# Performance work log

Measured on AMD Instinct MI355X. Metric: run time of the kernel, lower is better.

The kernel has to match this reference:

```python
import jax, jax.numpy as jnp
import numpy as np

VOCAB = 32000
LATENT = 1024
HID = 1024
LAYERS = 3
BATCH = 32
MAXLEN = 128


def setup_inputs() -> dict:
    key = jax.random.key(0)
    ks = jax.random.split(key, 10)
    s = 0.02
    return {
        "z": jax.random.normal(ks[0], (BATCH, LATENT), jnp.float32),
        "emb": jax.random.normal(ks[1], (VOCAB, LATENT), jnp.float32) * s,
        "w_lat": jax.random.normal(ks[2], (HID * LAYERS, LATENT), jnp.float32) * s,
        "b_lat": jnp.zeros((HID * LAYERS,), jnp.float32),
        "w_ih": jax.random.normal(ks[3], (LAYERS, 3 * HID, LATENT), jnp.float32) * s,
        "w_hh": jax.random.normal(ks[4], (LAYERS, 3 * HID, HID), jnp.float32) * s,
        "b_ih": jnp.zeros((LAYERS, 3 * HID), jnp.float32),
        "b_hh": jnp.zeros((LAYERS, 3 * HID), jnp.float32),
        "fc_w": jax.random.normal(ks[5], (VOCAB, HID), jnp.float32) * s,
        "fc_b": jnp.zeros((VOCAB,), jnp.float32),
        "max_length": MAXLEN,
    }


def _gru_cell(x, h, w_ih_l, w_hh_l, b_ih_l, b_hh_l):
    # x: [B, in], h: [B, H]; PyTorch GRU gate order: r, z, n
    gx = x @ w_ih_l.T + b_ih_l          # [B, 3H]
    gh = h @ w_hh_l.T + b_hh_l          # [B, 3H]
    xr, xz, xn = jnp.split(gx, 3, axis=-1)
    hr, hz, hn = jnp.split(gh, 3, axis=-1)
    r = jax.nn.sigmoid(xr + hr)
    zg = jax.nn.sigmoid(xz + hz)
    n = jnp.tanh(xn + r * hn)
    return (1.0 - zg) * n + zg * h


def reference(z, emb, w_lat, b_lat, w_ih, w_hh, b_ih, b_hh, fc_w, fc_b, max_length):
    B = z.shape[0]
    L, _, H = w_hh.shape
    # Faithful to source: hidden.view(num_layers, batch, hidden) on a [B, L*H] tensor
    hidden = (z @ w_lat.T + b_lat).reshape(L, B, H)
    tokens0 = jnp.zeros((B,), dtype=jnp.int32)

    def step(carry, _):
        tokens, h = carry
        x = emb[tokens]                          # [B, latent]
        new_h = []
        for l in range(L):                       # small fixed layer loop
            hl = _gru_cell(x, h[l], w_ih[l], w_hh[l], b_ih[l], b_hh[l])
            new_h.append(hl)
            x = hl
        h = jnp.stack(new_h)                     # [L, B, H]
        logits = x @ fc_w.T + fc_b               # [B, V]
        tokens = jnp.argmax(logits, axis=-1).astype(jnp.int32)
        return (tokens, h), logits

    _, logits_seq = jax.lax.scan(step, (tokens0, hidden), None, length=max_length)
    return jnp.transpose(logits_seq, (1, 0, 2))  # [B, T, V]
```

## Files before the change

### kernel.cpp

```cpp
#include <hip/hip_runtime.h>
#include <math.h>
#include <limits.h>

#define B32 32
#define KD 1024
#define HID 1024
#define VOC 32000
#define NL 3
#define TN 128
#define BKC 32
#define ASTR 36
#define WSTR 68
#define GEMM_THREADS 128
#define KS_GRU 4
#define CANDMAX 64

typedef __attribute__((ext_vector_type(8))) short bf16x8;
typedef __attribute__((ext_vector_type(8))) unsigned short u16x8;
typedef __attribute__((ext_vector_type(16))) float f32x16;

__device__ __forceinline__ float sigmoidf_(float x) { return 1.0f / (1.0f + expf(-x)); }

__device__ __forceinline__ unsigned short f2bf(float f) {
    unsigned u = __float_as_uint(f);
    u = u + 0x7fffu + ((u >> 16) & 1u);
    return (unsigned short)(u >> 16);
}
__device__ __forceinline__ float bf2f(unsigned short h) {
    return __uint_as_float(((unsigned)h) << 16);
}
__device__ __forceinline__ f32x16 MF(bf16x8 a, bf16x8 b, f32x16 c) {
    return __builtin_amdgcn_mfma_f32_32x32x16_bf16(a, b, c, 0, 0, 0);
}

__global__ __launch_bounds__(256)
void pack_w(const float* __restrict__ src, unsigned short* __restrict__ hi,
            unsigned short* __restrict__ lo, long ntiles)
{
    long tid = (long)blockIdx.x * 256 + threadIdx.x;
    long total = ntiles * 4096;
    if (tid >= total) return;
    long tile = tid >> 12;
    int r = (int)(tid & 4095);
    int k8 = r >> 5, c = r & 31;
    const float* s = src + ((size_t)tile * 32 + c) * KD + k8 * 8;
    float4 f0 = ((const float4*)s)[0];
    float4 f1 = ((const float4*)s)[1];
    float ff[8] = {f0.x, f0.y, f0.z, f0.w, f1.x, f1.y, f1.z, f1.w};
    u16x8 h, l;
#pragma unroll
    for (int j = 0; j < 8; ++j) {
        unsigned short hh = f2bf(ff[j]);
        h[j] = hh;
        l[j] = f2bf(ff[j] - bf2f(hh));
    }
    size_t o = ((size_t)tile << 15) + (size_t)k8 * 256 + (size_t)c * 8;
    *(u16x8*)(hi + o) = h;
    if (lo) *(u16x8*)(lo + o) = l;
}

__global__ __launch_bounds__(256)
void wnorm_k(const float* __restrict__ fcw, unsigned* __restrict__ wn)
{
    const int tid = threadIdx.x;
    const int r = blockIdx.x * 64 + (tid >> 2);
    const int q = tid & 3;
    const float* row = fcw + (size_t)r * KD + q * 256;
    float s = 0.f;
#pragma unroll 8
    for (int i = 0; i < 64; ++i) {
        float4 v = ((const float4*)row)[i];
        s += v.x * v.x + v.y * v.y + v.z * v.z + v.w * v.w;
    }
    s += __shfl_xor(s, 1);
    s += __shfl_xor(s, 2);
    if (q == 0) atomicMax(wn, __float_as_uint(sqrtf(s)));
}

__global__ __launch_bounds__(256)
void fix_gather(const float* __restrict__ out, int tprev, int T,
                const unsigned short* __restrict__ hh, const unsigned short* __restrict__ hl,
                const float* __restrict__ fcw, const float* __restrict__ fcb,
                const unsigned* __restrict__ wn,
                unsigned long long* __restrict__ wbuf,
                const float* __restrict__ emb,
                unsigned short* __restrict__ xhi, unsigned short* __restrict__ xlo,
                int do_fix)
{
    __shared__ float xs[1024];
    __shared__ float cval[CANDMAX];
    __shared__ int   cand[CANDMAX];
    __shared__ int   lcnt, stok;
    __shared__ float wsum[4];
    __shared__ float sred[4];
    const int b = blockIdx.x, tid = threadIdx.x;
    const int wv = tid >> 6, lane = tid & 63;

    if (do_fix) {
        if (tid == 0) lcnt = 0;
        float sq = 0.f;
        for (int k = tid; k < 1024; k += 256) {
            size_t hp = (size_t)(k >> 3) * 256 + (size_t)b * 8 + (k & 7);
            float xv = bf2f(hh[hp]) + bf2f(hl[hp]);
            xs[k] = xv;
            sq += xv * xv;
        }
#pragma unroll
        for (int m = 1; m < 64; m <<= 1) sq += __shfl_xor(sq, m);
        if (lane == 0) sred[wv] = sq;
        __syncthreads();
        float snorm = sred[0] + sred[1] + sred[2] + sred[3];
        unsigned long long key = wbuf[b];
        unsigned hi32 = (unsigned)(key >> 32);
        unsigned fb = (hi32 & 0x80000000u) ? (hi32 & 0x7fffffffu) : ~hi32;
        float m = __uint_as_float(fb);
        float delta = sqrtf(snorm) * __uint_as_float(wn[0]) * (1.01f / 256.0f) + 1e-7f;
        float thr = m - delta;
        const float* orow = out + ((size_t)b * T + tprev) * VOC;
        for (int i = tid; i < VOC / 4; i += 256) {
            float4 v = ((const float4*)orow)[i];
#pragma unroll
            for (int j = 0; j < 4; ++j) {
                float vv = ((const float*)&v)[j];
                if (vv >= thr) {
                    int pos = atomicAdd(&lcnt, 1);
                    if (pos < CANDMAX) cand[pos] = i * 4 + j;
                }
            }
        }
        __syncthreads();
        int nc = lcnt < CANDMAX ? lcnt : CANDMAX;
        for (int c = 0; c < nc; ++c) {
            const float* wr = fcw + (size_t)cand[c] * KD;
            float p = 0.f;
            for (int k = tid; k < 1024; k += 256) p += xs[k] * wr[k];
#pragma unroll
            for (int mm = 1; mm < 64; mm <<= 1) p += __shfl_xor(p, mm);
            if (lane == 0) wsum[wv] = p;
            __syncthreads();
            if (tid == 0) cval[c] = wsum[0] + wsum[1] + wsum[2] + wsum[3] + fcb[cand[c]];
            __syncthreads();
        }
        if (tid == 0) {
            float bv = -INFINITY; int bi = 0;
            for (int c = 0; c < nc; ++c) {
                float v = cval[c]; int ii = cand[c];
                if (c == 0 || v > bv || (v == bv && ii < bi)) { bv = v; bi = ii; }
            }
            stok = bi;
            wbuf[b] = 0ull;
        }
    }
    __syncthreads();
    int tok = do_fix ? stok : 0;
    if (tid < 128) {
        const float* er = emb + (size_t)tok * KD + (size_t)tid * 8;
        float4 f0 = ((const float4*)er)[0];
        float4 f1 = ((const float4*)er)[1];
        float ff[8] = {f0.x, f0.y, f0.z, f0.w, f1.x, f1.y, f1.z, f1.w};
        u16x8 h, l;
#pragma unroll
        for (int j = 0; j < 8; ++j) {
            unsigned short hv = f2bf(ff[j]);
            h[j] = hv;
            l[j] = f2bf(ff[j] - bf2f(hv));
        }
        size_t o = (size_t)tid * 256 + (size_t)b * 8;
        *(u16x8*)(xhi + o) = h;
        *(u16x8*)(xlo + o) = l;
    }
}

__global__ __launch_bounds__(384)
void gru_gemm(const unsigned short* __restrict__ xhi, const unsigned short* __restrict__ xlo,
              const unsigned short* __restrict__ hhi, const unsigned short* __restrict__ hlo,
              const unsigned short* __restrict__ wihhi, const unsigned short* __restrict__ wihlo,
              const unsigned short* __restrict__ whhhi, const unsigned short* __restrict__ whhlo,
              float* __restrict__ G)
{
    const int bid = blockIdx.x;
    const int jt = bid >> 2, ks4 = bid & 3;
    const int w = threadIdx.x >> 6, lane = threadIdx.x & 63;
    const int gate = (w < 3) ? w : w - 3;
    const unsigned short* Ah = (w < 3) ? xhi : hhi;
    const unsigned short* Al = (w < 3) ? xlo : hlo;
    const size_t woff = ((size_t)(gate * 32 + jt)) << 15;
    const unsigned short* Wh = ((w < 3) ? wihhi : whhhi) + woff;
    const unsigned short* Wl = ((w < 3) ? wihlo : whhlo) + woff;

    const size_t lo8 = (size_t)lane * 8;
    const int kbase = ks4 * 16;

    f32x16 acc = {0,0,0,0,0,0,0,0,0,0,0,0,0,0,0,0};
    bf16x8 ahB[4], alB[4], whB[4], wlB[4];
#pragma unroll
    for (int i = 0; i < 4; ++i) {
        size_t o = (size_t)(kbase + i) * 512 + lo8;
        ahB[i] = *(const bf16x8*)(Ah + o);
        alB[i] = *(const bf16x8*)(Al + o);
        whB[i] = *(const bf16x8*)(Wh + o);
        wlB[i] = *(const bf16x8*)(Wl + o);
    }
#pragma unroll
    for (int i = 0; i < 16; ++i) {
        const int s = i & 3;
        bf16x8 ah = ahB[s], al = alB[s], wh = whB[s], wl = wlB[s];
        if (i < 12) {
            size_t on = (size_t)(kbase + i + 4) * 512 + lo8;
            ahB[s] = *(const bf16x8*)(Ah + on);
            alB[s] = *(const bf16x8*)(Al + on);
            whB[s] = *(const bf16x8*)(Wh + on);
            wlB[s] = *(const bf16x8*)(Wl + on);
        }
        acc = MF(ah, wh, acc);
        acc = MF(al, wh, acc);
        acc = MF(ah, wl, acc);
    }

    const int kg = lane >> 5, c = lane & 31;
    float* Gb = G + (((size_t)(jt * 4 + ks4) * 6 + w) * B32) * 32;
#pragma unroll
    for (int r = 0; r < 16; ++r) {
        int b = (r & 3) + 8 * (r >> 2) + 4 * kg;
        Gb[b * 32 + c] = acc[r];
    }
}

__global__ __launch_bounds__(256)
void gru_gates2(const float* __restrict__ G,
                const float* __restrict__ bih, const float* __restrict__ bhh,
                unsigned short* __restrict__ hhi, unsigned short* __restrict__ hlo)
{
    int idx = blockIdx.x * 256 + threadIdx.x;
    int b = idx >> 10, j = idx & 1023;
    int jt = j >> 5, c = j & 31;
    float s0 = 0, s1 = 0, s2 = 0, s3 = 0, s4 = 0, s5 = 0;
#pragma unroll
    for (int ks = 0; ks < 4; ++ks) {
        const float* base = G + (((size_t)(jt * 4 + ks) * 6) * B32 + b) * 32 + c;
        s0 += base[0];
        s1 += base[1024];
        s2 += base[2048];
        s3 += base[3072];
        s4 += base[4096];
        s5 += base[5120];
    }
    float rg = sigmoidf_(s0 + bih[j] + s3 + bhh[j]);
    float zg = sigmoidf_(s1 + bih[KD + j] + s4 + bhh[KD + j]);
    float ng = tanhf(s2 + bih[2 * KD + j] + rg * (s5 + bhh[2 * KD + j]));
    size_t hp = (size_t)(j >> 3) * 256 + (size_t)b * 8 + (j & 7);
    float hold = bf2f(hhi[hp]) + bf2f(hlo[hp]);
    float hnew = (1.0f - zg) * ng + zg * hold;
    unsigned short hh = f2bf(hnew);
    hhi[hp] = hh;
    hlo[hp] = f2bf(hnew - bf2f(hh));
}

__global__ __launch_bounds__(256)
void logits6(const unsigned short* __restrict__ xh, const unsigned short* __restrict__ xl,
             const unsigned short* __restrict__ wh,
             const float* __restrict__ bias, float* __restrict__ out, int t, int T,
             unsigned long long* __restrict__ wbuf)
{
    __shared__ float bvalS[4][B32];
    __shared__ int   bidxS[4][B32];
    const int tid = threadIdx.x;
    const int w = tid >> 6, lane = tid & 63;
    const int tile = blockIdx.x * 4 + w;
    const int n0 = tile * 32;
    const unsigned short* Wt = wh + ((size_t)tile << 15);
    const size_t lo8 = (size_t)lane * 8;

    f32x16 acc = {0,0,0,0,0,0,0,0,0,0,0,0,0,0,0,0};
    bf16x8 ahB[4], alB[4], wvB[4];
#pragma unroll
    for (int i = 0; i < 4; ++i) {
        size_t o = (size_t)i * 512 + lo8;
        ahB[i] = *(const bf16x8*)(xh + o);
        alB[i] = *(const bf16x8*)(xl + o);
        wvB[i] = *(const bf16x8*)(Wt + o);
    }
#pragma unroll
    for (int i = 0; i < 64; ++i) {
        const int s = i & 3;
        bf16x8 ah = ahB[s], al = alB[s], wv = wvB[s];
        if (i < 60) {
            size_t on = (size_t)(i + 4) * 512 + lo8;
            ahB[s] = *(const bf16x8*)(xh + on);
            alB[s] = *(const bf16x8*)(xl + on);
            wvB[s] = *(const bf16x8*)(Wt + on);
        }
        acc = MF(ah, wv, acc);
        acc = MF(al, wv, acc);
    }

    const int kg = lane >> 5, col = lane & 31;
    const float bb = bias[n0 + col];
#pragma unroll
    for (int r = 0; r < 16; ++r) {
        int b = (r & 3) + 8 * (r >> 2) + 4 * kg;
        float v = acc[r] + bb;
        out[((size_t)b * T + t) * VOC + n0 + col] = v;
        float mv = v; int mi = n0 + col;
#pragma unroll
        for (int m = 1; m < 32; m <<= 1) {
            float ov = __shfl_xor(mv, m);
            int   oi = __shfl_xor(mi, m);
            if (ov > mv || (ov == mv && oi < mi)) { mv = ov; mi = oi; }
        }
        if (col == 0) { bvalS[w][b] = mv; bidxS[w][b] = mi; }
    }
    __syncthreads();
    if (tid < B32) {
        int b = tid;
        float mv = bvalS[0][b]; int mi = bidxS[0][b];
#pragma unroll
        for (int q = 1; q < 4; ++q) {
            float v = bvalS[q][b]; int ii = bidxS[q][b];
            if (v > mv || (v == mv && ii < mi)) { mv = v; mi = ii; }
        }
        unsigned u = __float_as_uint(mv);
        u = (u >> 31) ? ~u : (u | 0x80000000u);
        unsigned long long key =
            ((unsigned long long)u << 32) | (unsigned long long)(0xFFFFFFFFu - (unsigned)mi);
        atomicMax(wbuf + b, key);
    }
}

__global__ __launch_bounds__(GEMM_THREADS)
void gemm_k1024(const float* __restrict__ Ax, const float* __restrict__ Ah,
                const float* __restrict__ emb, const int* __restrict__ tokens, int gather0,
                const float* __restrict__ Wx, const float* __restrict__ Wh,
                const float* __restrict__ bias,
                float* __restrict__ C, int N, int KS)
{
    __shared__ float As[BKC * ASTR];
    __shared__ float Ws[2 * BKC * WSTR];
    const int tid = threadIdx.x;
    const int sel = blockIdx.y;
    const int ks  = blockIdx.x % KS;
    const int nt  = blockIdx.x / KS;
    const int n0  = nt * TN;
    const int klen = KD / KS;
    const int k0 = ks * klen;
    const float* A = sel ? Ah : Ax;
    const float* W = sel ? Wh : Wx;
    const bool gather = (sel == 0) && (gather0 != 0);

    const int tb = tid & 7;
    const int tn = tid >> 3;
    const int s_kq = tid & 7;
    const int s_r  = tid >> 3;

    const float* arow0;
    const float* arow1;
    if (gather) {
        arow0 = emb + (size_t)tokens[s_r] * KD;
        arow1 = emb + (size_t)tokens[s_r + 16] * KD;
    } else {
        arow0 = A + (size_t)s_r * KD;
        arow1 = A + (size_t)(s_r + 16) * KD;
    }
    const float* wrow = W + (size_t)(n0 + s_r) * KD;

    float acc[4][8];
#pragma unroll
    for (int i = 0; i < 4; ++i)
#pragma unroll
        for (int j = 0; j < 8; ++j) acc[i][j] = 0.0f;

    for (int kc = 0; kc < klen; kc += BKC) {
        const int kb = k0 + kc + s_kq * 4;
        float4 a0 = *(const float4*)(arow0 + kb);
        float4 a1 = *(const float4*)(arow1 + kb);
        float4 wv[8];
#pragma unroll
        for (int hh = 0; hh < 8; ++hh)
            wv[hh] = *(const float4*)(wrow + (size_t)hh * 16 * KD + kb);

        __syncthreads();
#pragma unroll
        for (int j = 0; j < 4; ++j) {
            As[(s_kq * 4 + j) * ASTR + s_r]      = ((const float*)&a0)[j];
            As[(s_kq * 4 + j) * ASTR + s_r + 16] = ((const float*)&a1)[j];
        }
#pragma unroll
        for (int hh = 0; hh < 8; ++hh) {
            int row = s_r + hh * 16;
            int half = row >> 6;
            int c = row & 63;
            float* wbase = &Ws[half * BKC * WSTR];
#pragma unroll
            for (int j = 0; j < 4; ++j)
                wbase[(s_kq * 4 + j) * WSTR + c] = ((const float*)&wv[hh])[j];
        }
        __syncthreads();

#pragma unroll
        for (int kk = 0; kk < BKC; ++kk) {
            float4 av = *(const float4*)&As[kk * ASTR + 4 * tb];
            float4 w0 = *(const float4*)&Ws[kk * WSTR + 4 * tn];
            float4 w1 = *(const float4*)&Ws[BKC * WSTR + kk * WSTR + 4 * tn];
#pragma unroll
            for (int i = 0; i < 4; ++i) {
                float a = ((const float*)&av)[i];
                acc[i][0] += a * w0.x; acc[i][1] += a * w0.y;
                acc[i][2] += a * w0.z; acc[i][3] += a * w0.w;
                acc[i][4] += a * w1.x; acc[i][5] += a * w1.y;
                acc[i][6] += a * w1.z; acc[i][7] += a * w1.w;
            }
        }
    }

    const int slice = sel * KS + ks;
    float* Cb = C + (size_t)slice * B32 * N;
    float4 bA = make_float4(0.f, 0.f, 0.f, 0.f), bB = bA;
    if (bias != nullptr && ks == 0) {
        bA = *(const float4*)&bias[n0 + 4 * tn];
        bB = *(const float4*)&bias[n0 + 64 + 4 * tn];
    }
#pragma unroll
    for (int i = 0; i < 4; ++i) {
        int b = 4 * tb + i;
        float4 vA = make_float4(acc[i][0] + bA.x, acc[i][1] + bA.y, acc[i][2] + bA.z, acc[i][3] + bA.w);
        float4 vB = make_float4(acc[i][4] + bB.x, acc[i][5] + bB.y, acc[i][6] + bB.z, acc[i][7] + bB.w);
        *(float4*)&Cb[(size_t)b * N + n0 + 4 * tn]       = vA;
        *(float4*)&Cb[(size_t)b * N + n0 + 64 + 4 * tn]  = vB;
    }
}

__global__ __launch_bounds__(256)
void gru_gates(const float* __restrict__ G,
               const float* __restrict__ bih, const float* __restrict__ bhh,
               float* __restrict__ hl)
{
    int idx = blockIdx.x * 256 + threadIdx.x;
    int b = idx >> 10, j = idx & 1023;
    float xr = 0, xz = 0, xn = 0, hr = 0, hz = 0, hn = 0;
#pragma unroll
    for (int ks = 0; ks < KS_GRU; ++ks) {
        const float* gx = G + ((size_t)ks * B32 + b) * 3072;
        const float* gh = G + ((size_t)(KS_GRU + ks) * B32 + b) * 3072;
        xr += gx[j];        xz += gx[1024 + j];  xn += gx[2048 + j];
        hr += gh[j];        hz += gh[1024 + j];  hn += gh[2048 + j];
    }
    float r = sigmoidf_(xr + bih[j] + hr + bhh[j]);
    float z = sigmoidf_(xz + bih[1024 + j] + hz + bhh[1024 + j]);
    float n = tanhf(xn + bih[2048 + j] + r * (hn + bhh[2048 + j]));
    float ho = hl[idx];
    hl[idx] = (1.0f - z) * n + z * ho;
}

__global__ __launch_bounds__(GEMM_THREADS)
void logits_kernel(const float* __restrict__ x,
                   const float* __restrict__ W, const float* __restrict__ bias,
                   float* __restrict__ out, int t, int T,
                   float* __restrict__ pval, int* __restrict__ pidx)
{
    __shared__ float As[BKC * ASTR];
    __shared__ float Ws[2 * BKC * WSTR];
    __shared__ float rval[B32 * 16];
    __shared__ int   ridx[B32 * 16];
    const int tid = threadIdx.x;
    const int n0 = blockIdx.x * TN;
    const int tb = tid & 7;
    const int tn = tid >> 3;
    const int s_kq = tid & 7;
    const int s_r  = tid >> 3;

    const float* arow0 = x + (size_t)s_r * KD;
    const float* arow1 = x + (size_t)(s_r + 16) * KD;
    const float* wrow  = W + (size_t)(n0 + s_r) * KD;

    float acc[4][8];
#pragma unroll
    for (int i = 0; i < 4; ++i)
#pragma unroll
        for (int j = 0; j < 8; ++j) acc[i][j] = 0.0f;

    for (int kc = 0; kc < KD; kc += BKC) {
        const int kb = kc + s_kq * 4;
        float4 a0 = *(const float4*)(arow0 + kb);
        float4 a1 = *(const float4*)(arow1 + kb);
        float4 wv[8];
#pragma unroll
        for (int hh = 0; hh < 8; ++hh)
            wv[hh] = *(const float4*)(wrow + (size_t)hh * 16 * KD + kb);

        __syncthreads();
#pragma unroll
        for (int j = 0; j < 4; ++j) {
            As[(s_kq * 4 + j) * ASTR + s_r]      = ((const float*)&a0)[j];
            As[(s_kq * 4 + j) * ASTR + s_r + 16] = ((const float*)&a1)[j];
        }
#pragma unroll
        for (int hh = 0; hh < 8; ++hh) {
            int row = s_r + hh * 16;
            int half = row >> 6;
            int c = row & 63;
            float* wbase = &Ws[half * BKC * WSTR];
#pragma unroll
            for (int j = 0; j < 4; ++j)
                wbase[(s_kq * 4 + j) * WSTR + c] = ((const float*)&wv[hh])[j];
        }
        __syncthreads();

#pragma unroll
        for (int kk = 0; kk < BKC; ++kk) {
            float4 av = *(const float4*)&As[kk * ASTR + 4 * tb];
            float4 w0 = *(const float4*)&Ws[kk * WSTR + 4 * tn];
            float4 w1 = *(const float4*)&Ws[BKC * WSTR + kk * WSTR + 4 * tn];
#pragma unroll
            for (int i = 0; i < 4; ++i) {
                float a = ((const float*)&av)[i];
                acc[i][0] += a * w0.x; acc[i][1] += a * w0.y;
                acc[i][2] += a * w0.z; acc[i][3] += a * w0.w;
                acc[i][4] += a * w1.x; acc[i][5] += a * w1.y;
                acc[i][6] += a * w1.z; acc[i][7] += a * w1.w;
            }
        }
    }

    float4 bA = *(const float4*)&bias[n0 + 4 * tn];
    float4 bB = *(const float4*)&bias[n0 + 64 + 4 * tn];

    float bestv[4]; int besti[4];
#pragma unroll
    for (int i = 0; i < 4; ++i) { bestv[i] = -INFINITY; besti[i] = INT_MAX; }

#pragma unroll
    for (int i = 0; i < 4; ++i) {
        int b = 4 * tb + i;
        float* orow = out + ((size_t)b * T + t) * VOC;
        float4 vA = make_float4(acc[i][0] + bA.x, acc[i][1] + bA.y, acc[i][2] + bA.z, acc[i][3] + bA.w);
        float4 vB = make_float4(acc[i][4] + bB.x, acc[i][5] + bB.y, acc[i][6] + bB.z, acc[i][7] + bB.w);
        *(float4*)&orow[n0 + 4 * tn]      = vA;
        *(float4*)&orow[n0 + 64 + 4 * tn] = vB;
#pragma unroll
        for (int j = 0; j < 4; ++j) {
            float v = ((const float*)&vA)[j]; int c = n0 + 4 * tn + j;
            if (v > bestv[i] || (v == bestv[i] && c < besti[i])) { bestv[i] = v; besti[i] = c; }
        }
#pragma unroll
        for (int j = 0; j < 4; ++j) {
            float v = ((const float*)&vB)[j]; int c = n0 + 64 + 4 * tn + j;
            if (v > bestv[i] || (v == bestv[i] && c < besti[i])) { bestv[i] = v; besti[i] = c; }
        }
    }
#pragma unroll
    for (int i = 0; i < 4; ++i) {
        rval[(4 * tb + i) * 16 + tn] = bestv[i];
        ridx[(4 * tb + i) * 16 + tn] = besti[i];
    }
    __syncthreads();
    if (tid < B32) {
        int b = tid;
        float bv = -INFINITY; int bi = INT_MAX;
        for (int q = 0; q < 16; ++q) {
            float v = rval[b * 16 + q]; int ii = ridx[b * 16 + q];
            if (v > bv || (v == bv && ii < bi)) { bv = v; bi = ii; }
        }
        pval[(size_t)blockIdx.x * B32 + b] = bv;
        pidx[(size_t)blockIdx.x * B32 + b] = bi;
    }
}

__global__ __launch_bounds__(256)
void amax_final(const float* __restrict__ pval, const int* __restrict__ pidx,
                int nblk, int* __restrict__ tokens)
{
    int tid = threadIdx.x;
    int b = tid >> 3, l8 = tid & 7;
    float bv = -INFINITY; int bi = INT_MAX;
    for (int q = l8; q < nblk; q += 8) {
        float v = pval[(size_t)q * B32 + b]; int ii = pidx[(size_t)q * B32 + b];
        if (v > bv || (v == bv && ii < bi)) { bv = v; bi = ii; }
    }
#pragma unroll
    for (int off = 1; off < 8; off <<= 1) {
        float ov = __shfl_xor(bv, off);
        int   oi = __shfl_xor(bi, off);
        if (ov > bv || (ov == bv && oi < bi)) { bv = ov; bi = oi; }
    }
    if (l8 == 0) tokens[b] = bi;
}

extern "C" void kernel_launch(void* const* d_in, const int* in_sizes, int n_in,
                              void* d_out, int out_size, void* d_ws, size_t ws_size,
                              hipStream_t stream)
{
    const float* z    = (const float*)d_in[0];
    const float* emb  = (const float*)d_in[1];
    const float* wlat = (const float*)d_in[2];
    const float* blat = (const float*)d_in[3];
    const float* wih  = (const float*)d_in[4];
    const float* whh  = (const float*)d_in[5];
    const float* bih  = (const float*)d_in[6];
    const float* bhh  = (const float*)d_in[7];
    const float* fcw  = (const float*)d_in[8];
    const float* fcb  = (const float*)d_in[9];
    float* out = (float*)d_out;
    const int T = out_size / (B32 * VOC);

    const size_t NEED = 152000000;
    if (ws_size >= NEED) {
        char* p = (char*)d_ws;
        auto take = [&](size_t bytes) { char* r = p; p += (bytes + 255) & ~(size_t)255; return r; };
        unsigned short* fcwPh = (unsigned short*)take((size_t)VOC * KD * 2);
        unsigned short* wihPh = (unsigned short*)take((size_t)NL * 3 * KD * KD * 2);
        unsigned short* wihPl = (unsigned short*)take((size_t)NL * 3 * KD * KD * 2);
        unsigned short* whhPh = (unsigned short*)take((size_t)NL * 3 * KD * KD * 2);
        unsigned short* whhPl = (unsigned short*)take((size_t)NL * 3 * KD * KD * 2);
        unsigned short* hPh   = (unsigned short*)take((size_t)NL * B32 * KD * 2);
        unsigned short* hPl   = (unsigned short*)take((size_t)NL * B32 * KD * 2);
        unsigned short* xPh   = (unsigned short*)take((size_t)B32 * KD * 2);
        unsigned short* xPl   = (unsigned short*)take((size_t)B32 * KD * 2);
        float* G   = (float*)take((size_t)32 * 4 * 6 * B32 * 32 * 4);
        float* h32 = (float*)take((size_t)B32 * NL * KD * 4);
        unsigned long long* wbuf = (unsigned long long*)take(B32 * 8);
        unsigned* wn = (unsigned*)take(256);

        hipMemsetAsync(wbuf, 0, B32 * 8, stream);
        hipMemsetAsync(wn, 0, 4, stream);

        {
            long nt_fc = VOC / 32;
            long nt_g  = (long)NL * 3 * KD / 32;
            pack_w<<<(unsigned)((nt_fc * 4096 + 255) / 256), 256, 0, stream>>>(fcw, fcwPh, nullptr, nt_fc);
            pack_w<<<(unsigned)((nt_g * 4096 + 255) / 256), 256, 0, stream>>>(wih, wihPh, wihPl, nt_g);
            pack_w<<<(unsigned)((nt_g * 4096 + 255) / 256), 256, 0, stream>>>(whh, whhPh, whhPl, nt_g);
            wnorm_k<<<VOC / 64, 256, 0, stream>>>(fcw, wn);
        }

        gemm_k1024<<<dim3(NL * KD / TN, 1), GEMM_THREADS, 0, stream>>>(
            z, nullptr, nullptr, nullptr, 0, wlat, nullptr, blat, h32, NL * KD, 1);
        pack_w<<<(unsigned)((3L * 4096 + 255) / 256), 256, 0, stream>>>(h32, hPh, hPl, 3);

        const size_t PL = (size_t)B32 * KD;
        for (int t = 0; t < T; ++t) {
            fix_gather<<<B32, 256, 0, stream>>>(
                out, t - 1, T, hPh + 2 * PL, hPl + 2 * PL, fcw, fcb, wn, wbuf,
                emb, xPh, xPl, t > 0 ? 1 : 0);

            for (int l = 0; l < NL; ++l) {
                const unsigned short* xh = (l == 0) ? xPh : hPh + (size_t)(l - 1) * PL;
                const unsigned short* xl = (l == 0) ? xPl : hPl + (size_t)(l - 1) * PL;
                gru_gemm<<<128, 384, 0, stream>>>(
                    xh, xl,
                    hPh + (size_t)l * PL, hPl + (size_t)l * PL,
                    wihPh + (size_t)l * 3 * KD * KD, wihPl + (size_t)l * 3 * KD * KD,
                    whhPh + (size_t)l * 3 * KD * KD, whhPl + (size_t)l * 3 * KD * KD,
                    G);
                gru_gates2<<<128, 256, 0, stream>>>(
                    G, bih + (size_t)l * 3 * KD, bhh + (size_t)l * 3 * KD,
                    hPh + (size_t)l * PL, hPl + (size_t)l * PL);
            }
            logits6<<<250, 256, 0, stream>>>(
                hPh + 2 * PL, hPl + 2 * PL, fcwPh, fcb, out, t, T, wbuf);
        }
    } else {
        float* h      = (float*)d_ws;
        float* G      = h + (size_t)B32 * NL * HID;
        float* pval   = G + (size_t)2 * KS_GRU * B32 * NL * HID;
        int*   pidx   = (int*)(pval + (VOC / TN) * B32);
        int*   tokens = (int*)(pidx + (VOC / TN) * B32);

        hipMemsetAsync(tokens, 0, B32 * sizeof(int), stream);

        gemm_k1024<<<dim3(NL * HID / TN, 1), GEMM_THREADS, 0, stream>>>(
            z, nullptr, nullptr, nullptr, 0, wlat, nullptr, blat, h, NL * HID, 1);

        for (int t = 0; t < T; ++t) {
            for (int l = 0; l < NL; ++l) {
                const float* xA = (l == 0) ? nullptr : (h + (size_t)(l - 1) * B32 * HID);
                dim3 gg((NL * HID / TN) * KS_GRU, 2);
                gemm_k1024<<<gg, GEMM_THREADS, 0, stream>>>(
                    xA, h + (size_t)l * B32 * HID, emb, tokens, (l == 0) ? 1 : 0,
                    wih + (size_t)l * NL * HID * KD, whh + (size_t)l * NL * HID * KD,
                    nullptr, G, NL * HID, KS_GRU);
                gru_gates<<<B32 * HID / 256, 256, 0, stream>>>(
                    G, bih + (size_t)l * NL * HID, bhh + (size_t)l * NL * HID,
                    h + (size_t)l * B32 * HID);
            }
            logits_kernel<<<VOC / TN, GEMM_THREADS, 0, stream>>>(
                h + (size_t)2 * B32 * HID, fcw, fcb, out, t, T, pval, pidx);
            amax_final<<<1, 256, 0, stream>>>(pval, pidx, VOC / TN, tokens);
        }
    }
}
```

Baseline: 10.88 ms.

## Fuse GRU gate epilogue into GEMM via last-block atomic counter, double-buffer hidden state

Merges the separate gate kernel into the GRU GEMM kernel. The last of the four K-split blocks for each 32-column tile, detected with an atomic counter, reduces the partials and applies the gate nonlinearities. The hidden state is ping-ponged between two buffers so the epilogue can write new h while other blocks still read old h. This removes three kernel launches per timestep. In exchange the reduction now runs on only 32 blocks and relies on threadfence-based cross-block ordering.

```diff
diff --git a/kernel.cpp b/kernel.cpp
--- a/kernel.cpp
+++ b/kernel.cpp
@@ -172,18 +172,22 @@
 }
 
 __global__ __launch_bounds__(384)
-void gru_gemm(const unsigned short* __restrict__ xhi, const unsigned short* __restrict__ xlo,
-              const unsigned short* __restrict__ hhi, const unsigned short* __restrict__ hlo,
-              const unsigned short* __restrict__ wihhi, const unsigned short* __restrict__ wihlo,
-              const unsigned short* __restrict__ whhhi, const unsigned short* __restrict__ whhlo,
-              float* __restrict__ G)
-{
+void gru_fused3(const unsigned short* __restrict__ xhi, const unsigned short* __restrict__ xlo,
+                const unsigned short* __restrict__ hch, const unsigned short* __restrict__ hcl,
+                unsigned short* __restrict__ hnh, unsigned short* __restrict__ hnl,
+                const unsigned short* __restrict__ wihhi, const unsigned short* __restrict__ wihlo,
+                const unsigned short* __restrict__ whhhi, const unsigned short* __restrict__ whhlo,
+                const float* __restrict__ bih, const float* __restrict__ bhh,
+                float* __restrict__ G, unsigned int* __restrict__ cnt)
+{
+    __shared__ int sflag;
     const int bid = blockIdx.x;
     const int jt = bid >> 2, ks4 = bid & 3;
-    const int w = threadIdx.x >> 6, lane = threadIdx.x & 63;
+    const int tid = threadIdx.x;
+    const int w = tid >> 6, lane = tid & 63;
     const int gate = (w < 3) ? w : w - 3;
-    const unsigned short* Ah = (w < 3) ? xhi : hhi;
-    const unsigned short* Al = (w < 3) ? xlo : hlo;
+    const unsigned short* Ah = (w < 3) ? xhi : hch;
+    const unsigned short* Al = (w < 3) ? xlo : hcl;
     const size_t woff = ((size_t)(gate * 32 + jt)) << 15;
     const unsigned short* Wh = ((w < 3) ? wihhi : whhhi) + woff;
     const unsigned short* Wl = ((w < 3) ? wihlo : whhlo) + woff;
@@ -224,36 +228,41 @@
         int b = (r & 3) + 8 * (r >> 2) + 4 * kg;
         Gb[b * 32 + c] = acc[r];
     }
-}
-
-__global__ __launch_bounds__(256)
-void gru_gates2(const float* __restrict__ G,
-                const float* __restrict__ bih, const float* __restrict__ bhh,
-                unsigned short* __restrict__ hhi, unsigned short* __restrict__ hlo)
-{
-    int idx = blockIdx.x * 256 + threadIdx.x;
-    int b = idx >> 10, j = idx & 1023;
-    int jt = j >> 5, c = j & 31;
-    float s0 = 0, s1 = 0, s2 = 0, s3 = 0, s4 = 0, s5 = 0;
-#pragma unroll
-    for (int ks = 0; ks < 4; ++ks) {
-        const float* base = G + (((size_t)(jt * 4 + ks) * 6) * B32 + b) * 32 + c;
-        s0 += base[0];
-        s1 += base[1024];
-        s2 += base[2048];
-        s3 += base[3072];
-        s4 += base[4096];
-        s5 += base[5120];
-    }
-    float rg = sigmoidf_(s0 + bih[j] + s3 + bhh[j]);
-    float zg = sigmoidf_(s1 + bih[KD + j] + s4 + bhh[KD + j]);
-    float ng = tanhf(s2 + bih[2 * KD + j] + rg * (s5 + bhh[2 * KD + j]));
-    size_t hp = (size_t)(j >> 3) * 256 + (size_t)b * 8 + (j & 7);
-    float hold = bf2f(hhi[hp]) + bf2f(hlo[hp]);
-    float hnew = (1.0f - zg) * ng + zg * hold;
-    unsigned short hh = f2bf(hnew);
-    hhi[hp] = hh;
-    hlo[hp] = f2bf(hnew - bf2f(hh));
+    __syncthreads();
+    if (tid == 0) {
+        __threadfence();
+        unsigned old = atomicAdd(&cnt[jt], 1u);
+        sflag = (old == 3) ? 1 : 0;
+        if (sflag) cnt[jt] = 0u;
+    }
+    __syncthreads();
+    if (sflag) {
+        __threadfence();
+        for (int idx = tid; idx < B32 * 32; idx += 384) {
+            int b = idx >> 5, c2 = idx & 31;
+            int j = jt * 32 + c2;
+            float s0 = 0, s1 = 0, s2 = 0, s3 = 0, s4 = 0, s5 = 0;
+#pragma unroll
+            for (int ks = 0; ks < 4; ++ks) {
+                const float* base = G + (((size_t)(jt * 4 + ks) * 6) * B32 + b) * 32 + c2;
+                s0 += base[0];
+                s1 += base[1024];
+                s2 += base[2048];
+                s3 += base[3072];
+                s4 += base[4096];
+                s5 += base[5120];
+            }
+            float rg = sigmoidf_(s0 + bih[j] + s3 + bhh[j]);
+            float zg = sigmoidf_(s1 + bih[KD + j] + s4 + bhh[KD + j]);
+            float ng = tanhf(s2 + bih[2 * KD + j] + rg * (s5 + bhh[2 * KD + j]));
+            size_t hp = (size_t)(j >> 3) * 256 + (size_t)b * 8 + (j & 7);
+            float hold = bf2f(hch[hp]) + bf2f(hcl[hp]);
+            float hnew = (1.0f - zg) * ng + zg * hold;
+            unsigned short hh = f2bf(hnew);
+            hnh[hp] = hh;
+            hnl[hp] = f2bf(hnew - bf2f(hh));
+        }
+    }
 }
 
 __global__ __launch_bounds__(256)
@@ -602,7 +611,7 @@
     float* out = (float*)d_out;
     const int T = out_size / (B32 * VOC);
 
-    const size_t NEED = 152000000;
+    const size_t NEED = 153000000;
     if (ws_size >= NEED) {
         char* p = (char*)d_ws;
         auto take = [&](size_t bytes) { char* r = p; p += (bytes + 255) & ~(size_t)255; return r; };
@@ -611,17 +620,21 @@
         unsigned short* wihPl = (unsigned short*)take((size_t)NL * 3 * KD * KD * 2);
         unsigned short* whhPh = (unsigned short*)take((size_t)NL * 3 * KD * KD * 2);
         unsigned short* whhPl = (unsigned short*)take((size_t)NL * 3 * KD * KD * 2);
-        unsigned short* hPh   = (unsigned short*)take((size_t)NL * B32 * KD * 2);
-        unsigned short* hPl   = (unsigned short*)take((size_t)NL * B32 * KD * 2);
+        unsigned short* hAh   = (unsigned short*)take((size_t)NL * B32 * KD * 2);
+        unsigned short* hAl   = (unsigned short*)take((size_t)NL * B32 * KD * 2);
+        unsigned short* hBh   = (unsigned short*)take((size_t)NL * B32 * KD * 2);
+        unsigned short* hBl   = (unsigned short*)take((size_t)NL * B32 * KD * 2);
         unsigned short* xPh   = (unsigned short*)take((size_t)B32 * KD * 2);
         unsigned short* xPl   = (unsigned short*)take((size_t)B32 * KD * 2);
         float* G   = (float*)take((size_t)32 * 4 * 6 * B32 * 32 * 4);
         float* h32 = (float*)take((size_t)B32 * NL * KD * 4);
         unsigned long long* wbuf = (unsigned long long*)take(B32 * 8);
         unsigned* wn = (unsigned*)take(256);
+        unsigned int* cnt = (unsigned int*)take(32 * 4);
 
         hipMemsetAsync(wbuf, 0, B32 * 8, stream);
         hipMemsetAsync(wn, 0, 4, stream);
+        hipMemsetAsync(cnt, 0, 32 * 4, stream);
 
         {
             long nt_fc = VOC / 32;
@@ -634,29 +647,33 @@
 
         gemm_k1024<<<dim3(NL * KD / TN, 1), GEMM_THREADS, 0, stream>>>(
             z, nullptr, nullptr, nullptr, 0, wlat, nullptr, blat, h32, NL * KD, 1);
-        pack_w<<<(unsigned)((3L * 4096 + 255) / 256), 256, 0, stream>>>(h32, hPh, hPl, 3);
+        pack_w<<<(unsigned)((3L * 4096 + 255) / 256), 256, 0, stream>>>(h32, hAh, hAl, 3);
 
         const size_t PL = (size_t)B32 * KD;
         for (int t = 0; t < T; ++t) {
+            unsigned short* ch = (t & 1) ? hBh : hAh;
+            unsigned short* cl = (t & 1) ? hBl : hAl;
+            unsigned short* nh = (t & 1) ? hAh : hBh;
+            unsigned short* nl = (t & 1) ? hAl : hBl;
+
             fix_gather<<<B32, 256, 0, stream>>>(
-                out, t - 1, T, hPh + 2 * PL, hPl + 2 * PL, fcw, fcb, wn, wbuf,
+                out, t - 1, T, ch + 2 * PL, cl + 2 * PL, fcw, fcb, wn, wbuf,
                 emb, xPh, xPl, t > 0 ? 1 : 0);
 
             for (int l = 0; l < NL; ++l) {
-                const unsigned short* xh = (l == 0) ? xPh : hPh + (size_t)(l - 1) * PL;
-                const unsigned short* xl = (l == 0) ? xPl : hPl + (size_t)(l - 1) * PL;
-                gru_gemm<<<128, 384, 0, stream>>>(
+                const unsigned short* xh = (l == 0) ? xPh : nh + (size_t)(l - 1) * PL;
+                const unsigned short* xl = (l == 0) ? xPl : nl + (size_t)(l - 1) * PL;
+                gru_fused3<<<128, 384, 0, stream>>>(
                     xh, xl,
-                    hPh + (size_t)l * PL, hPl + (size_t)l * PL,
+                    ch + (size_t)l * PL, cl + (size_t)l * PL,
+                    nh + (size_t)l * PL, nl + (size_t)l * PL,
                     wihPh + (size_t)l * 3 * KD * KD, wihPl + (size_t)l * 3 * KD * KD,
                     whhPh + (size_t)l * 3 * KD * KD, whhPl + (size_t)l * 3 * KD * KD,
-                    G);
-                gru_gates2<<<128, 256, 0, stream>>>(
-                    G, bih + (size_t)l * 3 * KD, bhh + (size_t)l * 3 * KD,
-                    hPh + (size_t)l * PL, hPl + (size_t)l * PL);
+                    bih + (size_t)l * 3 * KD, bhh + (size_t)l * 3 * KD,
+                    G, cnt);
             }
             logits6<<<250, 256, 0, stream>>>(
-                hPh + 2 * PL, hPl + 2 * PL, fcwPh, fcb, out, t, T, wbuf);
+                nh + 2 * PL, nl + 2 * PL, fcwPh, fcb, out, t, T, wbuf);
         }
     } else {
         float* h      = (float*)d_ws;
```

New measurement: 15.44 ms. 1.42x slower.

## Batch recurrent GEMMs across layers and fuse input GEMM with gate update

Applied to the files above, without the earlier changes.

The hidden-state GEMM (h @ W_hh) for all three layers is hoisted into one launch at the start of each step, since it depends only on the previous step's hidden state. The input GEMM is fused with the gate nonlinearity into a single kernel per layer that reduces partials in shared memory. This cuts per-step launches from 7 to 5 and takes the W_hh work off the serial layer chain. The cost is that the fused kernel runs only 32 blocks with K split in two, so each block does twice the K work and the GPU may be underused on that critical path.

```diff
diff --git a/kernel.cpp b/kernel.cpp
--- a/kernel.cpp
+++ b/kernel.cpp
@@ -171,25 +171,25 @@
     }
 }
 
-__global__ __launch_bounds__(384)
-void gru_gemm(const unsigned short* __restrict__ xhi, const unsigned short* __restrict__ xlo,
-              const unsigned short* __restrict__ hhi, const unsigned short* __restrict__ hlo,
-              const unsigned short* __restrict__ wihhi, const unsigned short* __restrict__ wihlo,
-              const unsigned short* __restrict__ whhhi, const unsigned short* __restrict__ whhlo,
-              float* __restrict__ G)
+__global__ __launch_bounds__(192)
+void gru_gh(const unsigned short* __restrict__ hPh, const unsigned short* __restrict__ hPl,
+            const unsigned short* __restrict__ whhPh, const unsigned short* __restrict__ whhPl,
+            float* __restrict__ Ggh)
 {
     const int bid = blockIdx.x;
-    const int jt = bid >> 2, ks4 = bid & 3;
+    const int l = bid >> 7;
+    const int r = bid & 127;
+    const int jt = r >> 2, ks = r & 3;
     const int w = threadIdx.x >> 6, lane = threadIdx.x & 63;
-    const int gate = (w < 3) ? w : w - 3;
-    const unsigned short* Ah = (w < 3) ? xhi : hhi;
-    const unsigned short* Al = (w < 3) ? xlo : hlo;
-    const size_t woff = ((size_t)(gate * 32 + jt)) << 15;
-    const unsigned short* Wh = ((w < 3) ? wihhi : whhhi) + woff;
-    const unsigned short* Wl = ((w < 3) ? wihlo : whhlo) + woff;
+    const size_t PL = (size_t)B32 * KD;
+    const unsigned short* Ah = hPh + (size_t)l * PL;
+    const unsigned short* Al = hPl + (size_t)l * PL;
+    const size_t woff = (size_t)l * 3 * KD * KD + (((size_t)(w * 32 + jt)) << 15);
+    const unsigned short* Wh = whhPh + woff;
+    const unsigned short* Wl = whhPl + woff;
 
     const size_t lo8 = (size_t)lane * 8;
-    const int kbase = ks4 * 16;
+    const int kbase = ks * 16;
 
     f32x16 acc = {0,0,0,0,0,0,0,0,0,0,0,0,0,0,0,0};
     bf16x8 ahB[4], alB[4], whB[4], wlB[4];
@@ -218,42 +218,90 @@
     }
 
     const int kg = lane >> 5, c = lane & 31;
-    float* Gb = G + (((size_t)(jt * 4 + ks4) * 6 + w) * B32) * 32;
-#pragma unroll
-    for (int r = 0; r < 16; ++r) {
-        int b = (r & 3) + 8 * (r >> 2) + 4 * kg;
-        Gb[b * 32 + c] = acc[r];
-    }
-}
-
-__global__ __launch_bounds__(256)
-void gru_gates2(const float* __restrict__ G,
-                const float* __restrict__ bih, const float* __restrict__ bhh,
-                unsigned short* __restrict__ hhi, unsigned short* __restrict__ hlo)
-{
-    int idx = blockIdx.x * 256 + threadIdx.x;
-    int b = idx >> 10, j = idx & 1023;
-    int jt = j >> 5, c = j & 31;
-    float s0 = 0, s1 = 0, s2 = 0, s3 = 0, s4 = 0, s5 = 0;
-#pragma unroll
-    for (int ks = 0; ks < 4; ++ks) {
-        const float* base = G + (((size_t)(jt * 4 + ks) * 6) * B32 + b) * 32 + c;
-        s0 += base[0];
-        s1 += base[1024];
-        s2 += base[2048];
-        s3 += base[3072];
-        s4 += base[4096];
-        s5 += base[5120];
-    }
-    float rg = sigmoidf_(s0 + bih[j] + s3 + bhh[j]);
-    float zg = sigmoidf_(s1 + bih[KD + j] + s4 + bhh[KD + j]);
-    float ng = tanhf(s2 + bih[2 * KD + j] + rg * (s5 + bhh[2 * KD + j]));
-    size_t hp = (size_t)(j >> 3) * 256 + (size_t)b * 8 + (j & 7);
-    float hold = bf2f(hhi[hp]) + bf2f(hlo[hp]);
-    float hnew = (1.0f - zg) * ng + zg * hold;
-    unsigned short hh = f2bf(hnew);
-    hhi[hp] = hh;
-    hlo[hp] = f2bf(hnew - bf2f(hh));
+    float* Gb = Ggh + (size_t)((l * 128 + jt * 4 + ks) * 3 + w) * 1024;
+#pragma unroll
+    for (int rr = 0; rr < 16; ++rr) {
+        int b = (rr & 3) + 8 * (rr >> 2) + 4 * kg;
+        Gb[b * 32 + c] = acc[rr];
+    }
+}
+
+__global__ __launch_bounds__(384)
+void gru_gx_gates(const unsigned short* __restrict__ xh, const unsigned short* __restrict__ xl,
+                  const unsigned short* __restrict__ wihh_l, const unsigned short* __restrict__ wihl_l,
+                  const float* __restrict__ Ggh_l,
+                  const float* __restrict__ bih_l, const float* __restrict__ bhh_l,
+                  unsigned short* __restrict__ hh_l, unsigned short* __restrict__ hl_l)
+{
+    __shared__ float gxs[2][3][B32][32];
+    const int jt = blockIdx.x;
+    const int tid = threadIdx.x;
+    const int w = tid >> 6, lane = tid & 63;
+    const int gate = (w < 3) ? w : w - 3;
+    const int kh = (w < 3) ? 0 : 1;
+    const unsigned short* Wh = wihh_l + (((size_t)(gate * 32 + jt)) << 15);
+    const unsigned short* Wl = wihl_l + (((size_t)(gate * 32 + jt)) << 15);
+    const size_t lo8 = (size_t)lane * 8;
+    const int kbase = kh * 32;
+
+    f32x16 acc = {0,0,0,0,0,0,0,0,0,0,0,0,0,0,0,0};
+    bf16x8 ahB[4], alB[4], whB[4], wlB[4];
+#pragma unroll
+    for (int i = 0; i < 4; ++i) {
+        size_t o = (size_t)(kbase + i) * 512 + lo8;
+        ahB[i] = *(const bf16x8*)(xh + o);
+        alB[i] = *(const bf16x8*)(xl + o);
+        whB[i] = *(const bf16x8*)(Wh + o);
+        wlB[i] = *(const bf16x8*)(Wl + o);
+    }
+#pragma unroll
+    for (int i = 0; i < 32; ++i) {
+        const int s = i & 3;
+        bf16x8 ah = ahB[s], al = alB[s], wh = whB[s], wl = wlB[s];
+        if (i < 28) {
+            size_t on = (size_t)(kbase + i + 4) * 512 + lo8;
+            ahB[s] = *(const bf16x8*)(xh + on);
+            alB[s] = *(const bf16x8*)(xl + on);
+            whB[s] = *(const bf16x8*)(Wh + on);
+            wlB[s] = *(const bf16x8*)(Wl + on);
+        }
+        acc = MF(ah, wh, acc);
+        acc = MF(al, wh, acc);
+        acc = MF(ah, wl, acc);
+    }
+
+    const int kg = lane >> 5, c = lane & 31;
+#pragma unroll
+    for (int rr = 0; rr < 16; ++rr) {
+        int b = (rr & 3) + 8 * (rr >> 2) + 4 * kg;
+        gxs[kh][gate][b][c] = acc[rr];
+    }
+    __syncthreads();
+
+    for (int idx = tid; idx < B32 * 32; idx += 384) {
+        int b = idx >> 5, c2 = idx & 31;
+        int j = jt * 32 + c2;
+        float g0 = gxs[0][0][b][c2] + gxs[1][0][b][c2];
+        float g1 = gxs[0][1][b][c2] + gxs[1][1][b][c2];
+        float g2 = gxs[0][2][b][c2] + gxs[1][2][b][c2];
+        float h0 = 0, h1 = 0, h2 = 0;
+#pragma unroll
+        for (int ks = 0; ks < 4; ++ks) {
+            const float* base = Ggh_l + (size_t)((jt * 4 + ks) * 3) * 1024 + b * 32 + c2;
+            h0 += base[0];
+            h1 += base[1024];
+            h2 += base[2048];
+        }
+        float rg = sigmoidf_(g0 + bih_l[j] + h0 + bhh_l[j]);
+        float zg = sigmoidf_(g1 + bih_l[KD + j] + h1 + bhh_l[KD + j]);
+        float ng = tanhf(g2 + bih_l[2 * KD + j] + rg * (h2 + bhh_l[2 * KD + j]));
+        size_t hp = (size_t)(j >> 3) * 256 + (size_t)b * 8 + (j & 7);
+        float hold = bf2f(hh_l[hp]) + bf2f(hl_l[hp]);
+        float hnew = (1.0f - zg) * ng + zg * hold;
+        unsigned short hh2 = f2bf(hnew);
+        hh_l[hp] = hh2;
+        hl_l[hp] = f2bf(hnew - bf2f(hh2));
+    }
 }
 
 __global__ __launch_bounds__(256)
@@ -615,7 +663,7 @@
         unsigned short* hPl   = (unsigned short*)take((size_t)NL * B32 * KD * 2);
         unsigned short* xPh   = (unsigned short*)take((size_t)B32 * KD * 2);
         unsigned short* xPl   = (unsigned short*)take((size_t)B32 * KD * 2);
-        float* G   = (float*)take((size_t)32 * 4 * 6 * B32 * 32 * 4);
+        float* Ggh = (float*)take((size_t)NL * 128 * 3 * 1024 * 4);
         float* h32 = (float*)take((size_t)B32 * NL * KD * 4);
         unsigned long long* wbuf = (unsigned long long*)take(B32 * 8);
         unsigned* wn = (unsigned*)take(256);
@@ -637,22 +685,22 @@
         pack_w<<<(unsigned)((3L * 4096 + 255) / 256), 256, 0, stream>>>(h32, hPh, hPl, 3);
 
         const size_t PL = (size_t)B32 * KD;
+        const size_t WL = (size_t)3 * KD * KD;
         for (int t = 0; t < T; ++t) {
             fix_gather<<<B32, 256, 0, stream>>>(
                 out, t - 1, T, hPh + 2 * PL, hPl + 2 * PL, fcw, fcb, wn, wbuf,
                 emb, xPh, xPl, t > 0 ? 1 : 0);
 
+            gru_gh<<<NL * 128, 192, 0, stream>>>(hPh, hPl, whhPh, whhPl, Ggh);
+
             for (int l = 0; l < NL; ++l) {
                 const unsigned short* xh = (l == 0) ? xPh : hPh + (size_t)(l - 1) * PL;
                 const unsigned short* xl = (l == 0) ? xPl : hPl + (size_t)(l - 1) * PL;
-                gru_gemm<<<128, 384, 0, stream>>>(
+                gru_gx_gates<<<32, 384, 0, stream>>>(
                     xh, xl,
-                    hPh + (size_t)l * PL, hPl + (size_t)l * PL,
-                    wihPh + (size_t)l * 3 * KD * KD, wihPl + (size_t)l * 3 * KD * KD,
-                    whhPh + (size_t)l * 3 * KD * KD, whhPl + (size_t)l * 3 * KD * KD,
-                    G);
-                gru_gates2<<<128, 256, 0, stream>>>(
-                    G, bih + (size_t)l * 3 * KD, bhh + (size_t)l * 3 * KD,
+                    wihPh + (size_t)l * WL, wihPl + (size_t)l * WL,
+                    Ggh + (size_t)l * 128 * 3 * 1024,
+                    bih + (size_t)l * 3 * KD, bhh + (size_t)l * 3 * KD,
                     hPh + (size_t)l * PL, hPl + (size_t)l * PL);
             }
             logits6<<<250, 256, 0, stream>>>(
```

Measured after the change: 13.30 ms. 22.2% more time.

## Hoist hidden-state GEMMs for all layers into the fix/gather kernel

Applied to the files above, without the earlier changes.

The h·W_hh products for all three layers depend only on the previous step's hidden state, so they are now computed up front in extra blocks of the fix/gather launch, running concurrently with the token fix and embedding gather. The per-layer GEMM then only computes the x·W_ih half with 192 threads, and the gates kernel reads the two partial buffers separately. This takes work off the serial per-layer chain of small launches and raises parallelism in the first kernel of each step. The cost is a larger buffer for the hidden-side partials and a heavier first launch.

```diff
diff --git a/kernel.cpp b/kernel.cpp
--- a/kernel.cpp
+++ b/kernel.cpp
@@ -78,21 +78,76 @@
 }
 
 __global__ __launch_bounds__(256)
-void fix_gather(const float* __restrict__ out, int tprev, int T,
-                const unsigned short* __restrict__ hh, const unsigned short* __restrict__ hl,
-                const float* __restrict__ fcw, const float* __restrict__ fcb,
-                const unsigned* __restrict__ wn,
-                unsigned long long* __restrict__ wbuf,
-                const float* __restrict__ emb,
-                unsigned short* __restrict__ xhi, unsigned short* __restrict__ xlo,
-                int do_fix)
-{
+void fix_gh(const float* __restrict__ out, int tprev, int T,
+            const unsigned short* __restrict__ hPh, const unsigned short* __restrict__ hPl,
+            const float* __restrict__ fcw, const float* __restrict__ fcb,
+            const unsigned* __restrict__ wn,
+            unsigned long long* __restrict__ wbuf,
+            const float* __restrict__ emb,
+            unsigned short* __restrict__ xhi, unsigned short* __restrict__ xlo,
+            const unsigned short* __restrict__ whhPh, const unsigned short* __restrict__ whhPl,
+            float* __restrict__ Ggh,
+            int do_fix)
+{
+    const size_t PL = (size_t)B32 * KD;
+    if (blockIdx.x >= B32) {
+        const int bid2 = blockIdx.x - B32;
+        const int l = bid2 >> 7;
+        const int r = bid2 & 127;
+        const int jt = r >> 2, ks = r & 3;
+        const int w = threadIdx.x >> 6, lane = threadIdx.x & 63;
+        if (w >= 3) return;
+        const unsigned short* Ah = hPh + (size_t)l * PL;
+        const unsigned short* Al = hPl + (size_t)l * PL;
+        const size_t woff = (size_t)l * 3 * KD * KD + (((size_t)(w * 32 + jt)) << 15);
+        const unsigned short* Wh = whhPh + woff;
+        const unsigned short* Wl = whhPl + woff;
+        const size_t lo8 = (size_t)lane * 8;
+        const int kbase = ks * 16;
+
+        f32x16 acc = {0,0,0,0,0,0,0,0,0,0,0,0,0,0,0,0};
+        bf16x8 ahB[4], alB[4], whB[4], wlB[4];
+#pragma unroll
+        for (int i = 0; i < 4; ++i) {
+            size_t o = (size_t)(kbase + i) * 512 + lo8;
+            ahB[i] = *(const bf16x8*)(Ah + o);
+            alB[i] = *(const bf16x8*)(Al + o);
+            whB[i] = *(const bf16x8*)(Wh + o);
+            wlB[i] = *(const bf16x8*)(Wl + o);
+        }
+#pragma unroll
+        for (int i = 0; i < 16; ++i) {
+            const int s = i & 3;
+            bf16x8 ah = ahB[s], al = alB[s], wh = whB[s], wl = wlB[s];
+            if (i < 12) {
+                size_t on = (size_t)(kbase + i + 4) * 512 + lo8;
+                ahB[s] = *(const bf16x8*)(Ah + on);
+                alB[s] = *(const bf16x8*)(Al + on);
+                whB[s] = *(const bf16x8*)(Wh + on);
+                wlB[s] = *(const bf16x8*)(Wl + on);
+            }
+            acc = MF(ah, wh, acc);
+            acc = MF(al, wh, acc);
+            acc = MF(ah, wl, acc);
+        }
+        const int kg = lane >> 5, c = lane & 31;
+        float* Gb = Ggh + ((size_t)(l * 128 + jt * 4 + ks) * 3 + w) * 1024;
+#pragma unroll
+        for (int rr = 0; rr < 16; ++rr) {
+            int b = (rr & 3) + 8 * (rr >> 2) + 4 * kg;
+            Gb[b * 32 + c] = acc[rr];
+        }
+        return;
+    }
+
     __shared__ float xs[1024];
     __shared__ float cval[CANDMAX];
     __shared__ int   cand[CANDMAX];
     __shared__ int   lcnt, stok;
     __shared__ float wsum[4];
     __shared__ float sred[4];
+    const unsigned short* hh = hPh + 2 * PL;
+    const unsigned short* hl = hPl + 2 * PL;
     const int b = blockIdx.x, tid = threadIdx.x;
     const int wv = tid >> 6, lane = tid & 63;
 
@@ -171,23 +226,17 @@
     }
 }
 
-__global__ __launch_bounds__(384)
-void gru_gemm(const unsigned short* __restrict__ xhi, const unsigned short* __restrict__ xlo,
-              const unsigned short* __restrict__ hhi, const unsigned short* __restrict__ hlo,
-              const unsigned short* __restrict__ wihhi, const unsigned short* __restrict__ wihlo,
-              const unsigned short* __restrict__ whhhi, const unsigned short* __restrict__ whhlo,
-              float* __restrict__ G)
+__global__ __launch_bounds__(192)
+void gru_gx(const unsigned short* __restrict__ xhi, const unsigned short* __restrict__ xlo,
+            const unsigned short* __restrict__ wihhi, const unsigned short* __restrict__ wihlo,
+            float* __restrict__ Gx)
 {
     const int bid = blockIdx.x;
     const int jt = bid >> 2, ks4 = bid & 3;
     const int w = threadIdx.x >> 6, lane = threadIdx.x & 63;
-    const int gate = (w < 3) ? w : w - 3;
-    const unsigned short* Ah = (w < 3) ? xhi : hhi;
-    const unsigned short* Al = (w < 3) ? xlo : hlo;
-    const size_t woff = ((size_t)(gate * 32 + jt)) << 15;
-    const unsigned short* Wh = ((w < 3) ? wihhi : whhhi) + woff;
-    const unsigned short* Wl = ((w < 3) ? wihlo : whhlo) + woff;
-
+    const size_t woff = ((size_t)(w * 32 + jt)) << 15;
+    const unsigned short* Wh = wihhi + woff;
+    const unsigned short* Wl = wihlo + woff;
     const size_t lo8 = (size_t)lane * 8;
     const int kbase = ks4 * 16;
 
@@ -196,8 +245,8 @@
 #pragma unroll
     for (int i = 0; i < 4; ++i) {
         size_t o = (size_t)(kbase + i) * 512 + lo8;
-        ahB[i] = *(const bf16x8*)(Ah + o);
-        alB[i] = *(const bf16x8*)(Al + o);
+        ahB[i] = *(const bf16x8*)(xhi + o);
+        alB[i] = *(const bf16x8*)(xlo + o);
         whB[i] = *(const bf16x8*)(Wh + o);
         wlB[i] = *(const bf16x8*)(Wl + o);
     }
@@ -207,8 +256,8 @@
         bf16x8 ah = ahB[s], al = alB[s], wh = whB[s], wl = wlB[s];
         if (i < 12) {
             size_t on = (size_t)(kbase + i + 4) * 512 + lo8;
-            ahB[s] = *(const bf16x8*)(Ah + on);
-            alB[s] = *(const bf16x8*)(Al + on);
+            ahB[s] = *(const bf16x8*)(xhi + on);
+            alB[s] = *(const bf16x8*)(xlo + on);
             whB[s] = *(const bf16x8*)(Wh + on);
             wlB[s] = *(const bf16x8*)(Wl + on);
         }
@@ -218,7 +267,7 @@
     }
 
     const int kg = lane >> 5, c = lane & 31;
-    float* Gb = G + (((size_t)(jt * 4 + ks4) * 6 + w) * B32) * 32;
+    float* Gb = Gx + ((size_t)((jt * 4 + ks4) * 3 + w)) * 1024;
 #pragma unroll
     for (int r = 0; r < 16; ++r) {
         int b = (r & 3) + 8 * (r >> 2) + 4 * kg;
@@ -227,7 +276,7 @@
 }
 
 __global__ __launch_bounds__(256)
-void gru_gates2(const float* __restrict__ G,
+void gru_gates3(const float* __restrict__ Gx, const float* __restrict__ Ggh_l,
                 const float* __restrict__ bih, const float* __restrict__ bhh,
                 unsigned short* __restrict__ hhi, unsigned short* __restrict__ hlo)
 {
@@ -237,13 +286,14 @@
     float s0 = 0, s1 = 0, s2 = 0, s3 = 0, s4 = 0, s5 = 0;
 #pragma unroll
     for (int ks = 0; ks < 4; ++ks) {
-        const float* base = G + (((size_t)(jt * 4 + ks) * 6) * B32 + b) * 32 + c;
-        s0 += base[0];
-        s1 += base[1024];
-        s2 += base[2048];
-        s3 += base[3072];
-        s4 += base[4096];
-        s5 += base[5120];
+        const float* bx = Gx    + ((size_t)((jt * 4 + ks) * 3)) * 1024 + b * 32 + c;
+        const float* bh = Ggh_l + ((size_t)((jt * 4 + ks) * 3)) * 1024 + b * 32 + c;
+        s0 += bx[0];
+        s1 += bx[1024];
+        s2 += bx[2048];
+        s3 += bh[0];
+        s4 += bh[1024];
+        s5 += bh[2048];
     }
     float rg = sigmoidf_(s0 + bih[j] + s3 + bhh[j]);
     float zg = sigmoidf_(s1 + bih[KD + j] + s4 + bhh[KD + j]);
@@ -615,7 +665,8 @@
         unsigned short* hPl   = (unsigned short*)take((size_t)NL * B32 * KD * 2);
         unsigned short* xPh   = (unsigned short*)take((size_t)B32 * KD * 2);
         unsigned short* xPl   = (unsigned short*)take((size_t)B32 * KD * 2);
-        float* G   = (float*)take((size_t)32 * 4 * 6 * B32 * 32 * 4);
+        float* Gx  = (float*)take((size_t)128 * 3 * 1024 * 4);
+        float* Ggh = (float*)take((size_t)NL * 128 * 3 * 1024 * 4);
         float* h32 = (float*)take((size_t)B32 * NL * KD * 4);
         unsigned long long* wbuf = (unsigned long long*)take(B32 * 8);
         unsigned* wn = (unsigned*)take(256);
@@ -637,22 +688,21 @@
         pack_w<<<(unsigned)((3L * 4096 + 255) / 256), 256, 0, stream>>>(h32, hPh, hPl, 3);
 
         const size_t PL = (size_t)B32 * KD;
+        const size_t WL = (size_t)3 * KD * KD;
         for (int t = 0; t < T; ++t) {
-            fix_gather<<<B32, 256, 0, stream>>>(
-                out, t - 1, T, hPh + 2 * PL, hPl + 2 * PL, fcw, fcb, wn, wbuf,
-                emb, xPh, xPl, t > 0 ? 1 : 0);
+            fix_gh<<<B32 + NL * 128, 256, 0, stream>>>(
+                out, t - 1, T, hPh, hPl, fcw, fcb, wn, wbuf,
+                emb, xPh, xPl, whhPh, whhPl, Ggh, t > 0 ? 1 : 0);
 
             for (int l = 0; l < NL; ++l) {
                 const unsigned short* xh = (l == 0) ? xPh : hPh + (size_t)(l - 1) * PL;
                 const unsigned short* xl = (l == 0) ? xPl : hPl + (size_t)(l - 1) * PL;
-                gru_gemm<<<128, 384, 0, stream>>>(
+                gru_gx<<<128, 192, 0, stream>>>(
                     xh, xl,
-                    hPh + (size_t)l * PL, hPl + (size_t)l * PL,
-                    wihPh + (size_t)l * 3 * KD * KD, wihPl + (size_t)l * 3 * KD * KD,
-                    whhPh + (size_t)l * 3 * KD * KD, whhPl + (size_t)l * 3 * KD * KD,
-                    G);
-                gru_gates2<<<128, 256, 0, stream>>>(
-                    G, bih + (size_t)l * 3 * KD, bhh + (size_t)l * 3 * KD,
+                    wihPh + (size_t)l * WL, wihPl + (size_t)l * WL, Gx);
+                gru_gates3<<<128, 256, 0, stream>>>(
+                    Gx, Ggh + (size_t)l * 128 * 3 * 1024,
+                    bih + (size_t)l * 3 * KD, bhh + (size_t)l * 3 * KD,
                     hPh + (size_t)l * PL, hPl + (size_t)l * PL);
             }
             logits6<<<250, 256, 0, stream>>>(
```

After: 10.81 ms. About the same (-0.7%).
